# Performance work log

Hardware: AMD Instinct MI355X
Metric: run time of the kernel (lower is better)

## Reference

```python
import jax, jax.numpy as jnp
import numpy as np

D_MODEL = 2048
NUM_EXPERTS = 64
TOP_K = 2
N_TOKENS = 16384


def setup_inputs() -> dict:
    key = jax.random.key(0)
    kx, kw = jax.random.split(key)
    x = jax.random.normal(kx, (N_TOKENS, D_MODEL), dtype=jnp.float32)
    # match nn.Linear default init scale roughly (not bit-exact; math is what matters)
    W = jax.random.normal(kw, (D_MODEL, NUM_EXPERTS), dtype=jnp.float32) * (1.0 / np.sqrt(D_MODEL))
    b = jnp.zeros((NUM_EXPERTS,), dtype=jnp.float32)
    return {"x": x, "W": W, "b": b}


def reference(x, W, b):
    # eval-mode forward (self.training False => no noise)
    logits = jnp.einsum("td,de->te", x, W) + b          # [T, E]
    weights = jax.nn.softmax(logits, axis=-1)             # [T, E]
    topk_weights, topk_indices = jax.lax.top_k(weights, TOP_K)  # [T, k] each
    return topk_weights, topk_indices, weights
```

## Files before the change

kernel.cpp:

```cpp
#include <hip/hip_runtime.h>
#include <math.h>


#define T_TOK 16384
#define DMOD  2048
#define NEXP  64
#define TM    64
#define NSL   4
#define DSL   (DMOD / NSL)
#define BK    32
#define NCH   (DSL / BK)
#define NT    512

__global__ __launch_bounds__(NT, 4) void gating_kernel(
    const float* __restrict__ x, const float* __restrict__ W,
    const float* __restrict__ bias, float* __restrict__ out) {
  __shared__ float smem[16384];
  float* xs = smem;
  float* wsm = smem + 8192;
  float* lg = smem;
  float* red_m = smem + 4160;
  float* red_s = smem + 4224;

  const int tid  = threadIdx.x;
  const int s    = tid >> 7;
  const int sl   = tid & 127;
  const int tg   = sl >> 4;
  const int eg   = sl & 15;
  const int tt   = sl >> 1;
  const int half = sl & 1;
  const int t0   = blockIdx.x * TM;

  const float* xg = x + (size_t)(t0 + tt) * DMOD + s * DSL + half * 16;
  const float* wg = W + (size_t)(s * DSL) * NEXP;
  float* xs_s = xs + s * 2048;
  float* ws_s = wsm + s * 2048;

  float acc[8][4];
#pragma unroll
  for (int i = 0; i < 8; ++i)
#pragma unroll
    for (int e = 0; e < 4; ++e) acc[i][e] = 0.f;

  for (int k = 0; k < NCH; ++k) {
    {
      const int kd = k * BK;
      float4 px[4], pw[4];
#pragma unroll
      for (int r = 0; r < 4; ++r) px[r] = *(const float4*)(xg + kd + r * 4);
#pragma unroll
      for (int r = 0; r < 4; ++r)
        pw[r] = ((const float4*)(wg + (size_t)kd * NEXP))[r * 128 + sl];
#pragma unroll
      for (int r = 0; r < 4; ++r) {
        const int d = half * 16 + r * 4;
        xs_s[(d + 0) * 64 + tt] = px[r].x;
        xs_s[(d + 1) * 64 + tt] = px[r].y;
        xs_s[(d + 2) * 64 + tt] = px[r].z;
        xs_s[(d + 3) * 64 + tt] = px[r].w;
        ((float4*)ws_s)[r * 128 + sl] = pw[r];
      }
    }
    __syncthreads();
#pragma unroll
    for (int j = 0; j < BK; ++j) {
      const float4 xa = *(const float4*)(xs_s + j * 64 + tg * 8);
      const float4 xb = *(const float4*)(xs_s + j * 64 + tg * 8 + 4);
      const float4 wv = *(const float4*)(ws_s + j * 64 + eg * 4);
      acc[0][0] = fmaf(xa.x, wv.x, acc[0][0]);
      acc[0][1] = fmaf(xa.x, wv.y, acc[0][1]);
      acc[0][2] = fmaf(xa.x, wv.z, acc[0][2]);
      acc[0][3] = fmaf(xa.x, wv.w, acc[0][3]);
      acc[1][0] = fmaf(xa.y, wv.x, acc[1][0]);
      acc[1][1] = fmaf(xa.y, wv.y, acc[1][1]);
      acc[1][2] = fmaf(xa.y, wv.z, acc[1][2]);
      acc[1][3] = fmaf(xa.y, wv.w, acc[1][3]);
      acc[2][0] = fmaf(xa.z, wv.x, acc[2][0]);
      acc[2][1] = fmaf(xa.z, wv.y, acc[2][1]);
      acc[2][2] = fmaf(xa.z, wv.z, acc[2][2]);
      acc[2][3] = fmaf(xa.z, wv.w, acc[2][3]);
      acc[3][0] = fmaf(xa.w, wv.x, acc[3][0]);
      acc[3][1] = fmaf(xa.w, wv.y, acc[3][1]);
      acc[3][2] = fmaf(xa.w, wv.z, acc[3][2]);
      acc[3][3] = fmaf(xa.w, wv.w, acc[3][3]);
      acc[4][0] = fmaf(xb.x, wv.x, acc[4][0]);
      acc[4][1] = fmaf(xb.x, wv.y, acc[4][1]);
      acc[4][2] = fmaf(xb.x, wv.z, acc[4][2]);
      acc[4][3] = fmaf(xb.x, wv.w, acc[4][3]);
      acc[5][0] = fmaf(xb.y, wv.x, acc[5][0]);
      acc[5][1] = fmaf(xb.y, wv.y, acc[5][1]);
      acc[5][2] = fmaf(xb.y, wv.z, acc[5][2]);
      acc[5][3] = fmaf(xb.y, wv.w, acc[5][3]);
      acc[6][0] = fmaf(xb.z, wv.x, acc[6][0]);
      acc[6][1] = fmaf(xb.z, wv.y, acc[6][1]);
      acc[6][2] = fmaf(xb.z, wv.z, acc[6][2]);
      acc[6][3] = fmaf(xb.z, wv.w, acc[6][3]);
      acc[7][0] = fmaf(xb.w, wv.x, acc[7][0]);
      acc[7][1] = fmaf(xb.w, wv.y, acc[7][1]);
      acc[7][2] = fmaf(xb.w, wv.z, acc[7][2]);
      acc[7][3] = fmaf(xb.w, wv.w, acc[7][3]);
    }
    __syncthreads();
  }

  {
    const float4 bv = *(const float4*)(bias + eg * 4);
#pragma unroll
    for (int ss = 0; ss < NSL; ++ss) {
      if (s == ss) {
#pragma unroll
        for (int i = 0; i < 8; ++i) {
          float* lrow = lg + (tg * 8 + i) * 65 + eg * 4;
          if (ss == 0) {
            lrow[0] = acc[i][0] + bv.x;
            lrow[1] = acc[i][1] + bv.y;
            lrow[2] = acc[i][2] + bv.z;
            lrow[3] = acc[i][3] + bv.w;
          } else {
            lrow[0] += acc[i][0];
            lrow[1] += acc[i][1];
            lrow[2] += acc[i][2];
            lrow[3] += acc[i][3];
          }
        }
      }
      __syncthreads();
    }
  }

  if (tid < TM) {
    float m = -INFINITY;
    for (int e = 0; e < NEXP; ++e) m = fmaxf(m, lg[tid * 65 + e]);
    float sum = 0.f, b1 = -INFINITY, b2 = -INFINITY;
    int i1 = 0, i2 = 0;
    for (int e = 0; e < NEXP; ++e) {
      const float v = lg[tid * 65 + e];
      sum += expf(v - m);
      if (v > b1) {
        b2 = b1; i2 = i1; b1 = v; i1 = e;
      } else if (v > b2) {
        b2 = v; i2 = e;
      }
    }
    const float inv = 1.f / sum;
    const int t = t0 + tid;
    out[2 * t + 0] = expf(b1 - m) * inv;
    out[2 * t + 1] = expf(b2 - m) * inv;
    out[2 * T_TOK + 2 * t + 0] = (float)i1;
    out[2 * T_TOK + 2 * t + 1] = (float)i2;
    red_m[tid] = m;
    red_s[tid] = inv;
  }
  __syncthreads();

#pragma unroll
  for (int r = 0; r < (TM * NEXP) / NT; ++r) {
    const int idx = r * NT + tid;
    const int ttk = idx >> 6;
    const int e = idx & 63;
    out[4 * T_TOK + (size_t)(t0 + ttk) * NEXP + e] =
        expf(lg[ttk * 65 + e] - red_m[ttk]) * red_s[ttk];
  }
}

extern "C" void kernel_launch(void* const* d_in, const int* in_sizes, int n_in,
                              void* d_out, int out_size, void* d_ws, size_t ws_size,
                              hipStream_t stream) {
  const float* x = (const float*)d_in[0];
  const float* W = (const float*)d_in[1];
  const float* b = (const float*)d_in[2];
  float* out = (float*)d_out;
  gating_kernel<<<dim3(T_TOK / TM), dim3(NT), 0, stream>>>(x, W, b, out);
}
```

Baseline: 236.8 us.

## Compute gating GEMM with bf16x3 split MFMA and register-prefetched loads

Replaces the FP32 FMA outer-product GEMM with matrix-core MFMA 16x16x32 bf16 instructions. Each fp32 value is split into three bf16 parts, and six cross products are accumulated to approximate fp32 precision. The K-split across four slices with a serial shared-memory reduction is removed, and the next chunk's global loads are prefetched into registers while the current chunk is computed. The cost is extra conversion ALU work on every tile load, plus precision that is only close to fp32, which can change near-tie top-k index choices.

```diff
diff --git a/kernel.cpp b/kernel.cpp
--- a/kernel.cpp
+++ b/kernel.cpp
@@ -6,136 +6,180 @@
 #define DMOD  2048
 #define NEXP  64
 #define TM    64
-#define NSL   4
-#define DSL   (DMOD / NSL)
-#define BK    32
-#define NCH   (DSL / BK)
+#define BK    64
+#define NCH   (DMOD / BK)
 #define NT    512
+#define LDK   72
+
+typedef __attribute__((ext_vector_type(8))) short short8;
+typedef __attribute__((ext_vector_type(4))) float f32x4;
+
+__device__ __forceinline__ unsigned short bf16_rne(float f) {
+  unsigned int u = __float_as_uint(f);
+  unsigned int r = (u + 0x7fffu + ((u >> 16) & 1u)) >> 16;
+  return (unsigned short)r;
+}
+__device__ __forceinline__ float bf16_up(unsigned short h) {
+  return __uint_as_float(((unsigned int)h) << 16);
+}
+__device__ __forceinline__ void split3(float v, unsigned short& h,
+                                       unsigned short& m, unsigned short& l) {
+  h = bf16_rne(v);
+  const float e1 = v - bf16_up(h);
+  m = bf16_rne(e1);
+  const float e2 = e1 - bf16_up(m);
+  l = bf16_rne(e2);
+}
 
 __global__ __launch_bounds__(NT, 4) void gating_kernel(
     const float* __restrict__ x, const float* __restrict__ W,
     const float* __restrict__ bias, float* __restrict__ out) {
-  __shared__ float smem[16384];
-  float* xs = smem;
-  float* wsm = smem + 8192;
-  float* lg = smem;
-  float* red_m = smem + 4160;
-  float* red_s = smem + 4224;
-
-  const int tid  = threadIdx.x;
-  const int s    = tid >> 7;
-  const int sl   = tid & 127;
-  const int tg   = sl >> 4;
-  const int eg   = sl & 15;
-  const int tt   = sl >> 1;
-  const int half = sl & 1;
-  const int t0   = blockIdx.x * TM;
-
-  const float* xg = x + (size_t)(t0 + tt) * DMOD + s * DSL + half * 16;
-  const float* wg = W + (size_t)(s * DSL) * NEXP;
-  float* xs_s = xs + s * 2048;
-  float* ws_s = wsm + s * 2048;
-
-  float acc[8][4];
-#pragma unroll
-  for (int i = 0; i < 8; ++i)
-#pragma unroll
-    for (int e = 0; e < 4; ++e) acc[i][e] = 0.f;
+  __shared__ __align__(16) unsigned short smem[6 * TM * LDK];
+  unsigned short* xs_h = smem;
+  unsigned short* xs_m = smem + TM * LDK;
+  unsigned short* xs_l = smem + 2 * TM * LDK;
+  unsigned short* wt_h = smem + 3 * TM * LDK;
+  unsigned short* wt_m = smem + 4 * TM * LDK;
+  unsigned short* wt_l = smem + 5 * TM * LDK;
+  float* lg    = (float*)smem;
+  float* red_m = (float*)smem + 4160;
+  float* red_s = (float*)smem + 4224;
+
+  const int tid = threadIdx.x;
+  const int l   = tid & 63;
+  const int w   = tid >> 6;
+  const int q   = l >> 4;
+  const int c   = l & 15;
+  const int t0  = blockIdx.x * TM;
+
+  const int xtok = tid >> 3;
+  const int xk0  = (tid & 7) * 8;
+  const int wn0  = (tid & 31) * 2;
+  const int wk0  = (tid >> 5) * 4;
+  const float* xg = x + (size_t)(t0 + xtok) * DMOD + xk0;
+  const float* wg = W + (size_t)wk0 * NEXP + wn0;
+
+  const int arow = (w & 3) * 16 + c;
+  const int bn0  = (w >> 2) * 32 + c;
+  const unsigned short* pa_h = xs_h + arow * LDK + q * 8;
+  const unsigned short* pa_m = xs_m + arow * LDK + q * 8;
+  const unsigned short* pa_l = xs_l + arow * LDK + q * 8;
+  const unsigned short* pb_h = wt_h + bn0 * LDK + q * 8;
+  const unsigned short* pb_m = wt_m + bn0 * LDK + q * 8;
+  const unsigned short* pb_l = wt_l + bn0 * LDK + q * 8;
+
+  f32x4 acc0 = {0.f, 0.f, 0.f, 0.f};
+  f32x4 acc1 = {0.f, 0.f, 0.f, 0.f};
+
+  float4 pxa, pxb;
+  float2 pwv[4];
+  pxa = *(const float4*)(xg);
+  pxb = *(const float4*)(xg + 4);
+#pragma unroll
+  for (int i = 0; i < 4; ++i) pwv[i] = *(const float2*)(wg + (size_t)i * NEXP);
 
   for (int k = 0; k < NCH; ++k) {
     {
-      const int kd = k * BK;
-      float4 px[4], pw[4];
-#pragma unroll
-      for (int r = 0; r < 4; ++r) px[r] = *(const float4*)(xg + kd + r * 4);
-#pragma unroll
-      for (int r = 0; r < 4; ++r)
-        pw[r] = ((const float4*)(wg + (size_t)kd * NEXP))[r * 128 + sl];
-#pragma unroll
-      for (int r = 0; r < 4; ++r) {
-        const int d = half * 16 + r * 4;
-        xs_s[(d + 0) * 64 + tt] = px[r].x;
-        xs_s[(d + 1) * 64 + tt] = px[r].y;
-        xs_s[(d + 2) * 64 + tt] = px[r].z;
-        xs_s[(d + 3) * 64 + tt] = px[r].w;
-        ((float4*)ws_s)[r * 128 + sl] = pw[r];
+      float xv[8] = {pxa.x, pxa.y, pxa.z, pxa.w, pxb.x, pxb.y, pxb.z, pxb.w};
+      unsigned short h[8], m[8], lo[8];
+#pragma unroll
+      for (int j = 0; j < 8; ++j) split3(xv[j], h[j], m[j], lo[j]);
+      uint4 hp, mp, lp;
+      hp.x = (unsigned)h[0] | ((unsigned)h[1] << 16);
+      hp.y = (unsigned)h[2] | ((unsigned)h[3] << 16);
+      hp.z = (unsigned)h[4] | ((unsigned)h[5] << 16);
+      hp.w = (unsigned)h[6] | ((unsigned)h[7] << 16);
+      mp.x = (unsigned)m[0] | ((unsigned)m[1] << 16);
+      mp.y = (unsigned)m[2] | ((unsigned)m[3] << 16);
+      mp.z = (unsigned)m[4] | ((unsigned)m[5] << 16);
+      mp.w = (unsigned)m[6] | ((unsigned)m[7] << 16);
+      lp.x = (unsigned)lo[0] | ((unsigned)lo[1] << 16);
+      lp.y = (unsigned)lo[2] | ((unsigned)lo[3] << 16);
+      lp.z = (unsigned)lo[4] | ((unsigned)lo[5] << 16);
+      lp.w = (unsigned)lo[6] | ((unsigned)lo[7] << 16);
+      *(uint4*)(xs_h + xtok * LDK + xk0) = hp;
+      *(uint4*)(xs_m + xtok * LDK + xk0) = mp;
+      *(uint4*)(xs_l + xtok * LDK + xk0) = lp;
+#pragma unroll
+      for (int n = 0; n < 2; ++n) {
+        unsigned short wh[4], wm[4], wl[4];
+#pragma unroll
+        for (int i = 0; i < 4; ++i) {
+          const float v = n == 0 ? pwv[i].x : pwv[i].y;
+          split3(v, wh[i], wm[i], wl[i]);
+        }
+        uint2 hp2, mp2, lp2;
+        hp2.x = (unsigned)wh[0] | ((unsigned)wh[1] << 16);
+        hp2.y = (unsigned)wh[2] | ((unsigned)wh[3] << 16);
+        mp2.x = (unsigned)wm[0] | ((unsigned)wm[1] << 16);
+        mp2.y = (unsigned)wm[2] | ((unsigned)wm[3] << 16);
+        lp2.x = (unsigned)wl[0] | ((unsigned)wl[1] << 16);
+        lp2.y = (unsigned)wl[2] | ((unsigned)wl[3] << 16);
+        *(uint2*)(wt_h + (wn0 + n) * LDK + wk0) = hp2;
+        *(uint2*)(wt_m + (wn0 + n) * LDK + wk0) = mp2;
+        *(uint2*)(wt_l + (wn0 + n) * LDK + wk0) = lp2;
       }
     }
     __syncthreads();
-#pragma unroll
-    for (int j = 0; j < BK; ++j) {
-      const float4 xa = *(const float4*)(xs_s + j * 64 + tg * 8);
-      const float4 xb = *(const float4*)(xs_s + j * 64 + tg * 8 + 4);
-      const float4 wv = *(const float4*)(ws_s + j * 64 + eg * 4);
-      acc[0][0] = fmaf(xa.x, wv.x, acc[0][0]);
-      acc[0][1] = fmaf(xa.x, wv.y, acc[0][1]);
-      acc[0][2] = fmaf(xa.x, wv.z, acc[0][2]);
-      acc[0][3] = fmaf(xa.x, wv.w, acc[0][3]);
-      acc[1][0] = fmaf(xa.y, wv.x, acc[1][0]);
-      acc[1][1] = fmaf(xa.y, wv.y, acc[1][1]);
-      acc[1][2] = fmaf(xa.y, wv.z, acc[1][2]);
-      acc[1][3] = fmaf(xa.y, wv.w, acc[1][3]);
-      acc[2][0] = fmaf(xa.z, wv.x, acc[2][0]);
-      acc[2][1] = fmaf(xa.z, wv.y, acc[2][1]);
-      acc[2][2] = fmaf(xa.z, wv.z, acc[2][2]);
-      acc[2][3] = fmaf(xa.z, wv.w, acc[2][3]);
-      acc[3][0] = fmaf(xa.w, wv.x, acc[3][0]);
-      acc[3][1] = fmaf(xa.w, wv.y, acc[3][1]);
-      acc[3][2] = fmaf(xa.w, wv.z, acc[3][2]);
-      acc[3][3] = fmaf(xa.w, wv.w, acc[3][3]);
-      acc[4][0] = fmaf(xb.x, wv.x, acc[4][0]);
-      acc[4][1] = fmaf(xb.x, wv.y, acc[4][1]);
-      acc[4][2] = fmaf(xb.x, wv.z, acc[4][2]);
-      acc[4][3] = fmaf(xb.x, wv.w, acc[4][3]);
-      acc[5][0] = fmaf(xb.y, wv.x, acc[5][0]);
-      acc[5][1] = fmaf(xb.y, wv.y, acc[5][1]);
-      acc[5][2] = fmaf(xb.y, wv.z, acc[5][2]);
-      acc[5][3] = fmaf(xb.y, wv.w, acc[5][3]);
-      acc[6][0] = fmaf(xb.z, wv.x, acc[6][0]);
-      acc[6][1] = fmaf(xb.z, wv.y, acc[6][1]);
-      acc[6][2] = fmaf(xb.z, wv.z, acc[6][2]);
-      acc[6][3] = fmaf(xb.z, wv.w, acc[6][3]);
-      acc[7][0] = fmaf(xb.w, wv.x, acc[7][0]);
-      acc[7][1] = fmaf(xb.w, wv.y, acc[7][1]);
-      acc[7][2] = fmaf(xb.w, wv.z, acc[7][2]);
-      acc[7][3] = fmaf(xb.w, wv.w, acc[7][3]);
+
+    if (k + 1 < NCH) {
+      const int kc = (k + 1) * BK;
+      pxa = *(const float4*)(xg + kc);
+      pxb = *(const float4*)(xg + kc + 4);
+#pragma unroll
+      for (int i = 0; i < 4; ++i)
+        pwv[i] = *(const float2*)(wg + (size_t)(kc + i) * NEXP);
+    }
+
+#pragma unroll
+    for (int s = 0; s < 2; ++s) {
+      const int ko = s * 32;
+      const short8 a_h = *(const short8*)(pa_h + ko);
+      const short8 a_m = *(const short8*)(pa_m + ko);
+      const short8 a_l = *(const short8*)(pa_l + ko);
+      const short8 b_h0 = *(const short8*)(pb_h + ko);
+      const short8 b_m0 = *(const short8*)(pb_m + ko);
+      const short8 b_l0 = *(const short8*)(pb_l + ko);
+      const short8 b_h1 = *(const short8*)(pb_h + 16 * LDK + ko);
+      const short8 b_m1 = *(const short8*)(pb_m + 16 * LDK + ko);
+      const short8 b_l1 = *(const short8*)(pb_l + 16 * LDK + ko);
+      acc0 = __builtin_amdgcn_mfma_f32_16x16x32_bf16(a_h, b_h0, acc0, 0, 0, 0);
+      acc0 = __builtin_amdgcn_mfma_f32_16x16x32_bf16(a_h, b_m0, acc0, 0, 0, 0);
+      acc0 = __builtin_amdgcn_mfma_f32_16x16x32_bf16(a_m, b_h0, acc0, 0, 0, 0);
+      acc0 = __builtin_amdgcn_mfma_f32_16x16x32_bf16(a_m, b_m0, acc0, 0, 0, 0);
+      acc0 = __builtin_amdgcn_mfma_f32_16x16x32_bf16(a_h, b_l0, acc0, 0, 0, 0);
+      acc0 = __builtin_amdgcn_mfma_f32_16x16x32_bf16(a_l, b_h0, acc0, 0, 0, 0);
+      acc1 = __builtin_amdgcn_mfma_f32_16x16x32_bf16(a_h, b_h1, acc1, 0, 0, 0);
+      acc1 = __builtin_amdgcn_mfma_f32_16x16x32_bf16(a_h, b_m1, acc1, 0, 0, 0);
+      acc1 = __builtin_amdgcn_mfma_f32_16x16x32_bf16(a_m, b_h1, acc1, 0, 0, 0);
+      acc1 = __builtin_amdgcn_mfma_f32_16x16x32_bf16(a_m, b_m1, acc1, 0, 0, 0);
+      acc1 = __builtin_amdgcn_mfma_f32_16x16x32_bf16(a_h, b_l1, acc1, 0, 0, 0);
+      acc1 = __builtin_amdgcn_mfma_f32_16x16x32_bf16(a_l, b_h1, acc1, 0, 0, 0);
     }
     __syncthreads();
   }
 
   {
-    const float4 bv = *(const float4*)(bias + eg * 4);
-#pragma unroll
-    for (int ss = 0; ss < NSL; ++ss) {
-      if (s == ss) {
-#pragma unroll
-        for (int i = 0; i < 8; ++i) {
-          float* lrow = lg + (tg * 8 + i) * 65 + eg * 4;
-          if (ss == 0) {
-            lrow[0] = acc[i][0] + bv.x;
-            lrow[1] = acc[i][1] + bv.y;
-            lrow[2] = acc[i][2] + bv.z;
-            lrow[3] = acc[i][3] + bv.w;
-          } else {
-            lrow[0] += acc[i][0];
-            lrow[1] += acc[i][1];
-            lrow[2] += acc[i][2];
-            lrow[3] += acc[i][3];
-          }
-        }
-      }
-      __syncthreads();
-    }
-  }
+    const int row0 = (w & 3) * 16 + q * 4;
+    const int e0 = (w >> 2) * 32 + c;
+    const float bv0 = bias[e0];
+    const float bv1 = bias[e0 + 16];
+#pragma unroll
+    for (int r = 0; r < 4; ++r) {
+      lg[(row0 + r) * 65 + e0] = acc0[r] + bv0;
+      lg[(row0 + r) * 65 + e0 + 16] = acc1[r] + bv1;
+    }
+  }
+  __syncthreads();
 
   if (tid < TM) {
-    float m = -INFINITY;
-    for (int e = 0; e < NEXP; ++e) m = fmaxf(m, lg[tid * 65 + e]);
+    float mx = -INFINITY;
+    for (int e = 0; e < NEXP; ++e) mx = fmaxf(mx, lg[tid * 65 + e]);
     float sum = 0.f, b1 = -INFINITY, b2 = -INFINITY;
     int i1 = 0, i2 = 0;
     for (int e = 0; e < NEXP; ++e) {
       const float v = lg[tid * 65 + e];
-      sum += expf(v - m);
+      sum += expf(v - mx);
       if (v > b1) {
         b2 = b1; i2 = i1; b1 = v; i1 = e;
       } else if (v > b2) {
@@ -144,11 +188,11 @@
     }
     const float inv = 1.f / sum;
     const int t = t0 + tid;
-    out[2 * t + 0] = expf(b1 - m) * inv;
-    out[2 * t + 1] = expf(b2 - m) * inv;
+    out[2 * t + 0] = expf(b1 - mx) * inv;
+    out[2 * t + 1] = expf(b2 - mx) * inv;
     out[2 * T_TOK + 2 * t + 0] = (float)i1;
     out[2 * T_TOK + 2 * t + 1] = (float)i2;
-    red_m[tid] = m;
+    red_m[tid] = mx;
     red_s[tid] = inv;
   }
   __syncthreads();
@@ -156,10 +200,10 @@
 #pragma unroll
   for (int r = 0; r < (TM * NEXP) / NT; ++r) {
     const int idx = r * NT + tid;
-    const int ttk = idx >> 6;
+    const int tt = idx >> 6;
     const int e = idx & 63;
-    out[4 * T_TOK + (size_t)(t0 + ttk) * NEXP + e] =
-        expf(lg[ttk * 65 + e] - red_m[ttk]) * red_s[ttk];
+    out[4 * T_TOK + (size_t)(t0 + tt) * NEXP + e] =
+        expf(lg[tt * 65 + e] - red_m[tt]) * red_s[tt];
   }
 }
 
```

Measured after the change: 227.6 us. 3.9% less time.
